# Optimization experiments

Measured on AMD Instinct MI355X. Metric: run time of the kernel, lower is better.

The kernel has to match this reference:

```python
import jax, jax.numpy as jnp
from jax import lax
import numpy as np

BATCH = 524288
SEQ_LEN = 64


def setup_inputs() -> dict:
    key = jax.random.key(0)
    ka, kb = jax.random.split(key)
    a = jax.random.randint(ka, (BATCH, SEQ_LEN), 0, 10).astype(jnp.float32)
    b = jax.random.randint(kb, (BATCH, SEQ_LEN), 0, 10).astype(jnp.float32)
    # RNNCell params as hardcoded in Adder._initialize_weights
    weight_ih = jnp.array([[1.0, 1.0]], dtype=jnp.float32)   # (hidden=1, input=2)
    weight_hh = jnp.array([[1.0]], dtype=jnp.float32)        # (1, 1)
    bias_ih = jnp.zeros((1,), dtype=jnp.float32)
    bias_hh = jnp.zeros((1,), dtype=jnp.float32)
    return {"a": a, "b": b, "weight_ih": weight_ih, "weight_hh": weight_hh,
            "bias_ih": bias_ih, "bias_hh": bias_hh}


def reference(a, b, weight_ih, weight_hh, bias_ih, bias_hh):
    # a, b: (B, S) base-10 digits; carry h: (B, 1) hidden state.
    # Process digits from least significant (rightmost) to most significant.
    xs = jnp.stack([a, b], axis=-1)            # (B, S, 2)
    xs = jnp.flip(xs, axis=1)                  # reversed digit order
    xs = jnp.swapaxes(xs, 0, 1)                # (S, B, 2) for scan

    def step(h, x):
        # RNNCell with relu: u = relu(x @ W_ih^T + b_ih + h @ W_hh^T + b_hh)
        u = jax.nn.relu(x @ weight_ih.T + bias_ih + h @ weight_hh.T + bias_hh)  # (B,1)
        carry = jax.nn.relu(u - 9.0) - jax.nn.relu(u - 10.0)                    # (B,1)
        s = x[:, 0] + x[:, 1] + h[:, 0]                                         # (B,)
        digit = s - 10.0 * carry[:, 0]                                          # (B,)
        return carry, digit

    h0 = jnp.zeros((a.shape[0], 1), dtype=a.dtype)
    _, digits_rev = lax.scan(step, h0, xs)     # (S, B), least-significant first
    digits = jnp.flip(digits_rev, axis=0).T    # (B, S), original order
    return digits
```

## Files before the change

### kernel.cpp

```cpp
#include <hip/hip_runtime.h>


__global__ __launch_bounds__(256) void adder_kernel(
    const float* __restrict__ a,
    const float* __restrict__ b,
    float* __restrict__ out,
    long long n_rows)
{
    const int lane = (int)(threadIdx.x & 63);
    const long long row = (long long)blockIdx.x * 4 + (threadIdx.x >> 6);
    if (row >= n_rows) return;

    const long long idx = row * 64 + lane;
    const float s = a[idx] + b[idx];

    const unsigned long long g_l = __ballot(s >= 10.0f);
    const unsigned long long p_l = __ballot(s == 9.0f);

    const unsigned long long G  = __brevll(g_l);
    const unsigned long long P  = __brevll(p_l);
    const unsigned long long PG = P | G;
    const unsigned long long C_pos = (PG + G) ^ PG ^ G;
    const unsigned long long C_l   = __brevll(C_pos);

    const float cin = (float)((C_l >> lane) & 1ULL);
    const float u = s + cin;
    const float carry_out = (u >= 10.0f) ? 1.0f : 0.0f;
    out[idx] = u - 10.0f * carry_out;
}

extern "C" void kernel_launch(void* const* d_in, const int* in_sizes, int n_in,
                              void* d_out, int out_size, void* d_ws, size_t ws_size,
                              hipStream_t stream) {
    const float* a = (const float*)d_in[0];
    const float* b = (const float*)d_in[1];
    float* out = (float*)d_out;

    const long long n_rows = (long long)in_sizes[0] / 64;
    const int blocks = (int)((n_rows + 3) / 4);
    adder_kernel<<<blocks, 256, 0, stream>>>(a, b, out, n_rows);
}
```

Baseline: 308.6 us.

## Process four rows per wave with float4 loads and hierarchical carry lookahead

Each lane now loads four consecutive digits with 128-bit vector loads, so one wave covers four 64-digit rows. Carry generate/propagate is computed per 4-digit group, then combined across 16-lane row segments through a ballot and a 16-bit carry-lookahead add. Output is written with nontemporal 128-bit stores. This aims to cut memory-instruction count and improve bandwidth use on a memory-bound kernel, but it drops the row bounds check and assumes the row count is a multiple of 16.

```diff
diff --git a/kernel.cpp b/kernel.cpp
--- a/kernel.cpp
+++ b/kernel.cpp
@@ -1,32 +1,62 @@
 #include <hip/hip_runtime.h>
 
+
+typedef float f32x4 __attribute__((ext_vector_type(4)));
 
 __global__ __launch_bounds__(256) void adder_kernel(
     const float* __restrict__ a,
     const float* __restrict__ b,
-    float* __restrict__ out,
-    long long n_rows)
+    float* __restrict__ out)
 {
     const int lane = (int)(threadIdx.x & 63);
-    const long long row = (long long)blockIdx.x * 4 + (threadIdx.x >> 6);
-    if (row >= n_rows) return;
+    const long long wave = (long long)blockIdx.x * 4 + (threadIdx.x >> 6);
 
-    const long long idx = row * 64 + lane;
-    const float s = a[idx] + b[idx];
+    const long long base = wave * 256 + 4 * lane;
 
-    const unsigned long long g_l = __ballot(s >= 10.0f);
-    const unsigned long long p_l = __ballot(s == 9.0f);
+    const f32x4 av = *(const f32x4*)(a + base);
+    const f32x4 bv = *(const f32x4*)(b + base);
 
-    const unsigned long long G  = __brevll(g_l);
-    const unsigned long long P  = __brevll(p_l);
-    const unsigned long long PG = P | G;
-    const unsigned long long C_pos = (PG + G) ^ PG ^ G;
-    const unsigned long long C_l   = __brevll(C_pos);
+    const float s0 = av.x + bv.x;
+    const float s1 = av.y + bv.y;
+    const float s2 = av.z + bv.z;
+    const float s3 = av.w + bv.w;
 
-    const float cin = (float)((C_l >> lane) & 1ULL);
-    const float u = s + cin;
-    const float carry_out = (u >= 10.0f) ? 1.0f : 0.0f;
-    out[idx] = u - 10.0f * carry_out;
+    const unsigned g4 = (unsigned)(s3 >= 10.0f)
+                      | ((unsigned)(s2 >= 10.0f) << 1)
+                      | ((unsigned)(s1 >= 10.0f) << 2)
+                      | ((unsigned)(s0 >= 10.0f) << 3);
+    const unsigned p4 = (unsigned)(s3 == 9.0f)
+                      | ((unsigned)(s2 == 9.0f) << 1)
+                      | ((unsigned)(s1 == 9.0f) << 2)
+                      | ((unsigned)(s0 == 9.0f) << 3);
+    const unsigned pg4 = p4 | g4;
+    const unsigned c4  = (pg4 + g4) ^ pg4 ^ g4;
+    const bool Ggrp = (c4 >> 4) & 1u;
+    const bool Pgrp = (p4 == 0xFu);
+
+    const unsigned long long Gl = __ballot(Ggrp);
+    const unsigned long long Pl = __ballot(Pgrp);
+
+    const int r = lane >> 4;
+    const int j = lane & 15;
+
+    unsigned Gr = (unsigned)((Gl >> (16 * r)) & 0xFFFFull);
+    unsigned Pr = (unsigned)((Pl >> (16 * r)) & 0xFFFFull);
+    Gr = __brev(Gr) >> 16;
+    Pr = __brev(Pr) >> 16;
+    const unsigned PGr = Pr | Gr;
+    const unsigned Cr  = (PGr + Gr) ^ PGr ^ Gr;
+
+    const float cin = (float)((Cr >> (15 - j)) & 1u);
+
+    float u, c;
+    f32x4 d;
+    u = s3 + cin; c = (u >= 10.0f) ? 1.0f : 0.0f; d.w = u - 10.0f * c;
+    u = s2 + c;   c = (u >= 10.0f) ? 1.0f : 0.0f; d.z = u - 10.0f * c;
+    u = s1 + c;   c = (u >= 10.0f) ? 1.0f : 0.0f; d.y = u - 10.0f * c;
+    u = s0 + c;   c = (u >= 10.0f) ? 1.0f : 0.0f; d.x = u - 10.0f * c;
+
+    __builtin_nontemporal_store(d, (f32x4*)(out + base));
 }
 
 extern "C" void kernel_launch(void* const* d_in, const int* in_sizes, int n_in,
@@ -37,6 +67,6 @@
     float* out = (float*)d_out;
 
     const long long n_rows = (long long)in_sizes[0] / 64;
-    const int blocks = (int)((n_rows + 3) / 4);
-    adder_kernel<<<blocks, 256, 0, stream>>>(a, b, out, n_rows);
+    const int blocks = (int)(n_rows / 16);
+    adder_kernel<<<blocks, 256, 0, stream>>>(a, b, out);
 }
```

Result: slower. 318.5 us (+3.2%).
